# Optimization experiments

Measured on AMD Instinct MI355X. Metric: run time of the kernel, lower is better.

The kernel has to match this reference:

```python
import jax, jax.numpy as jnp
import numpy as np

NHEAD = 16


def setup_inputs() -> dict:
    key = jax.random.key(0)
    ks = jax.random.split(key, 8)
    B, T, C = 2, 1024, 2048
    H, D = NHEAD, C // NHEAD
    P = 1024  # past kv length
    s = 0.02
    return {
        "x": jax.random.normal(ks[0], (B, T, C), jnp.float32),
        "past_k": jax.random.normal(ks[1], (B, H, P, D), jnp.float32),
        "past_v": jax.random.normal(ks[2], (B, H, P, D), jnp.float32),
        "Wk": jax.random.normal(ks[3], (C, C), jnp.float32) * s,
        "Wq": jax.random.normal(ks[4], (C, C), jnp.float32) * s,
        "Wv": jax.random.normal(ks[5], (C, C), jnp.float32) * s,
        "Wp": jax.random.normal(ks[6], (C, C), jnp.float32) * s,
        "bp": jax.random.normal(ks[7], (C,), jnp.float32) * s,
    }


def reference(x, past_k, past_v, Wk, Wq, Wv, Wp, bp):
    B, T, C = x.shape
    H = NHEAD
    D = C // H
    # nn.Linear(W): y = x @ W.T ; split into heads -> [B,H,T,D]
    def proj_heads(W):
        return (x @ W.T).reshape(B, T, H, D).transpose(0, 2, 1, 3)
    q = proj_heads(Wq)
    k_new = proj_heads(Wk)
    v_new = proj_heads(Wv)
    k = jnp.concatenate([past_k, k_new], axis=2)  # [B,H,P+T,D]
    v = jnp.concatenate([past_v, v_new], axis=2)
    past_len = past_k.shape[2]
    total_len = past_len + T
    # causal mask: new-query row i attends to absolute position j <= past_len + i
    q_pos = past_len + jnp.arange(T)[:, None]        # [T,1]
    k_pos = jnp.arange(total_len)[None, :]           # [1,total]
    mask = k_pos <= q_pos                            # [T,total]
    att = jnp.einsum("bhqd,bhkd->bhqk", q, k) * (1.0 / np.sqrt(D).astype(np.float32))
    att = jnp.where(mask[None, None], att, jnp.float32(-jnp.inf))
    att = jax.nn.softmax(att, axis=-1)
    out = jnp.einsum("bhqk,bhkd->bhqd", att, v)
    out = out.transpose(0, 2, 1, 3).reshape(B, T, C)
    out = out @ Wp.T + bp
    return out, k, v
```

## Files before the change

kernel.cpp:

```cpp
#include <hip/hip_runtime.h>
#include <stdint.h>

#define B_ 2
#define T_ 1024
#define C_ 2048
#define H_ 16
#define D_ 128
#define P_ 1024
#define L_ 2048
#define M_ 2048

typedef unsigned short u16;
typedef __attribute__((ext_vector_type(8))) short short8;
typedef __attribute__((ext_vector_type(4))) float f32x4;
typedef __attribute__((ext_vector_type(8))) u16 u16x8;
typedef __attribute__((ext_vector_type(4))) u16 u16x4;

__device__ __forceinline__ u16 f2bf(float x) {
    union { float f; uint32_t u; } c; c.f = x;
    uint32_t u = c.u;
    return (u16)((u + 0x7fffu + ((u >> 16) & 1u)) >> 16);
}

__device__ __forceinline__ void gload_lds16(const void* g, void* l) {
    typedef __attribute__((address_space(1))) const void gvoid;
    typedef __attribute__((address_space(3))) void lvoid;
    __builtin_amdgcn_global_load_lds((gvoid*)g, (lvoid*)l, 16, 0, 0);
}

__global__ __launch_bounds__(256) void convert4_kernel(
        const float* __restrict__ x,  const float* __restrict__ wk,
        const float* __restrict__ wv, const float* __restrict__ wq,
        u16* __restrict__ xb, u16* __restrict__ obK,
        u16* __restrict__ obV, u16* __restrict__ obQ) {
    const int bid = blockIdx.x;
    const int r = bid >> 11;
    const int i = (bid & 2047) * 256 + threadIdx.x;
    const float* src = (r == 0) ? x : (r == 1) ? wk : (r == 2) ? wv : wq;
    u16* dst = (r == 0) ? xb : (r == 1) ? obK : (r == 2) ? obV : obQ;
    float4 a = ((const float4*)src)[i * 2], b = ((const float4*)src)[i * 2 + 1];
    ((u16x8*)dst)[i] = u16x8{f2bf(a.x), f2bf(a.y), f2bf(a.z), f2bf(a.w),
                             f2bf(b.x), f2bf(b.y), f2bf(b.z), f2bf(b.w)};
}

__global__ __launch_bounds__(256) void convert_bf16_kernel(
        const float* __restrict__ in, u16* __restrict__ out) {
    int i = blockIdx.x * 256 + threadIdx.x;
    const float4* p = (const float4*)in;
    float4 a = p[i * 2], b = p[i * 2 + 1];
    ((u16x8*)out)[i] = u16x8{f2bf(a.x), f2bf(a.y), f2bf(a.z), f2bf(a.w),
                             f2bf(b.x), f2bf(b.y), f2bf(b.z), f2bf(b.w)};
}

__global__ __launch_bounds__(256) void copy_past_kernel(
        const float4* __restrict__ pk, const float4* __restrict__ pv,
        float4* __restrict__ kdst, float4* __restrict__ vdst,
        u16x4* __restrict__ kb) {
    int i = blockIdx.x * 256 + threadIdx.x;
    int bh = i >> 15;
    int rest = i & 32767;
    size_t dst = (size_t)bh * (L_ * D_ / 4) + rest;
    float4 k4 = pk[i], v4 = pv[i];
    kdst[dst] = k4;
    vdst[dst] = v4;
    kb[dst] = u16x4{f2bf(k4.x), f2bf(k4.y), f2bf(k4.z), f2bf(k4.w)};
}

__global__ __launch_bounds__(256) void vT_past_kernel(
        const float* __restrict__ pv, u16* __restrict__ vbT) {
    __shared__ float s[64][65];
    const int tid = threadIdx.x;
    const int bh = blockIdx.x >> 5;
    const int tile = blockIdx.x & 31;
    const int k0 = (tile >> 1) * 64;
    const int d0 = (tile & 1) * 64;
    const float* src = pv + ((size_t)bh * P_ + k0) * D_ + d0;
    {
        int r = tid >> 2, c0 = (tid & 3) * 16;
#pragma unroll
        for (int u = 0; u < 4; ++u) {
            float4 f = *(const float4*)(src + (size_t)r * D_ + c0 + u * 4);
            s[r][c0 + u * 4 + 0] = f.x; s[r][c0 + u * 4 + 1] = f.y;
            s[r][c0 + u * 4 + 2] = f.z; s[r][c0 + u * 4 + 3] = f.w;
        }
    }
    __syncthreads();
    int d = tid >> 2, ck = (tid & 3) * 16;
    u16* dst = vbT + ((size_t)bh * D_ + d0 + d) * L_ + k0 + ck;
    u16x8 o0, o1;
#pragma unroll
    for (int j = 0; j < 8; ++j) o0[j] = f2bf(s[ck + j][d]);
#pragma unroll
    for (int j = 0; j < 8; ++j) o1[j] = f2bf(s[ck + 8 + j][d]);
    *(u16x8*)dst = o0;
    *(u16x8*)(dst + 8) = o1;
}

__global__ __launch_bounds__(256) void gemm_qkv(
        const u16* __restrict__ A,
        const u16* __restrict__ wbK, const u16* __restrict__ wbV,
        const u16* __restrict__ wbQ,
        float* __restrict__ kout, float* __restrict__ vout,
        u16* __restrict__ kb, u16* __restrict__ vbT, u16* __restrict__ Qst) {
    __shared__ u16 As[128 * 32];
    __shared__ u16 Bs[128 * 32];
    const int tid  = threadIdx.x;
    const int wave = tid >> 6;
    const int lane = tid & 63;
    const int m0   = blockIdx.y * 128;
    const int n0g  = blockIdx.x * 128;
    const int region = n0g >> 11;
    const int n0   = n0g & 2047;
    const u16* Bw = (region == 0) ? wbK : (region == 1) ? wbV : wbQ;

    f32x4 acc[4][4];
#pragma unroll
    for (int i = 0; i < 4; ++i)
#pragma unroll
        for (int j = 0; j < 4; ++j) acc[i][j] = f32x4{0.f, 0.f, 0.f, 0.f};

    const int srow = lane >> 2;
    const int scol = (lane & 3) * 8;
    const int q0 = wave * 2, q1 = wave * 2 + 1;
    const u16* A0 = A  + (size_t)(m0 + q0 * 16 + srow) * C_ + scol;
    const u16* A1 = A  + (size_t)(m0 + q1 * 16 + srow) * C_ + scol;
    const u16* B0 = Bw + (size_t)(n0 + q0 * 16 + srow) * C_ + scol;
    const u16* B1 = Bw + (size_t)(n0 + q1 * 16 + srow) * C_ + scol;

    const int frow = lane & 15;
    const int fko  = (lane >> 4) * 8;
    const int wr = (wave >> 1) * 64;
    const int wc = (wave & 1) * 64;

    for (int kt = 0; kt < C_; kt += 32) {
        __syncthreads();
        gload_lds16(A0 + kt, &As[q0 * 512]);
        gload_lds16(A1 + kt, &As[q1 * 512]);
        gload_lds16(B0 + kt, &Bs[q0 * 512]);
        gload_lds16(B1 + kt, &Bs[q1 * 512]);
        __syncthreads();
        short8 af[4], bf[4];
#pragma unroll
        for (int i = 0; i < 4; ++i) {
            af[i] = *(const short8*)&As[(wr + i * 16 + frow) * 32 + fko];
            bf[i] = *(const short8*)&Bs[(wc + i * 16 + frow) * 32 + fko];
        }
#pragma unroll
        for (int mi = 0; mi < 4; ++mi)
#pragma unroll
            for (int ni = 0; ni < 4; ++ni)
                acc[mi][ni] = __builtin_amdgcn_mfma_f32_16x16x32_bf16(
                    af[mi], bf[ni], acc[mi][ni], 0, 0, 0);
    }

    const int ccol = lane & 15;
    const int crb  = (lane >> 4) * 4;
#pragma unroll
    for (int mi = 0; mi < 4; ++mi) {
#pragma unroll
        for (int ni = 0; ni < 4; ++ni) {
            const int gc  = n0 + wc + ni * 16 + ccol;
            const int grb = m0 + wr + mi * 16 + crb;
            if (region == 2) {
#pragma unroll
                for (int r = 0; r < 4; ++r)
                    Qst[(size_t)(grb + r) * C_ + gc] = f2bf(acc[mi][ni][r]);
            } else {
                const int b = grb >> 10, tb = grb & 1023;
                const int h = gc >> 7,  d  = gc & 127;
                const size_t fb = (((size_t)(b * H_ + h)) * L_ + P_ + tb) * D_ + d;
                if (region == 0) {
#pragma unroll
                    for (int r = 0; r < 4; ++r) {
                        kout[fb + (size_t)r * D_] = acc[mi][ni][r];
                        kb[fb + (size_t)r * D_]   = f2bf(acc[mi][ni][r]);
                    }
                } else {
#pragma unroll
                    for (int r = 0; r < 4; ++r) vout[fb + (size_t)r * D_] = acc[mi][ni][r];
                    const size_t tb2 = (((size_t)(b * H_ + h)) * D_ + d) * L_ + P_ + tb;
                    *(u16x4*)&vbT[tb2] = u16x4{
                        f2bf(acc[mi][ni][0]), f2bf(acc[mi][ni][1]),
                        f2bf(acc[mi][ni][2]), f2bf(acc[mi][ni][3])};
                }
            }
        }
    }
}

template <int MODE>
__global__ __launch_bounds__(256) void gemm128(
        const u16* __restrict__ A, const u16* __restrict__ Bw,
        float* __restrict__ outf, u16* __restrict__ outb,
        const float* __restrict__ bias) {
    __shared__ u16 As[128 * 32];
    __shared__ u16 Bs[128 * 32];
    const int tid  = threadIdx.x;
    const int wave = tid >> 6;
    const int lane = tid & 63;
    const int m0 = blockIdx.y * 128;
    const int n0 = blockIdx.x * 128;

    f32x4 acc[4][4];
#pragma unroll
    for (int i = 0; i < 4; ++i)
#pragma unroll
        for (int j = 0; j < 4; ++j) acc[i][j] = f32x4{0.f, 0.f, 0.f, 0.f};

    const int srow = lane >> 2;
    const int scol = (lane & 3) * 8;
    const int q0 = wave * 2, q1 = wave * 2 + 1;
    const u16* A0 = A  + (size_t)(m0 + q0 * 16 + srow) * C_ + scol;
    const u16* A1 = A  + (size_t)(m0 + q1 * 16 + srow) * C_ + scol;
    const u16* B0 = Bw + (size_t)(n0 + q0 * 16 + srow) * C_ + scol;
    const u16* B1 = Bw + (size_t)(n0 + q1 * 16 + srow) * C_ + scol;

    const int frow = lane & 15;
    const int fko  = (lane >> 4) * 8;
    const int wr = (wave >> 1) * 64;
    const int wc = (wave & 1) * 64;

    for (int kt = 0; kt < C_; kt += 32) {
        __syncthreads();
        gload_lds16(A0 + kt, &As[q0 * 512]);
        gload_lds16(A1 + kt, &As[q1 * 512]);
        gload_lds16(B0 + kt, &Bs[q0 * 512]);
        gload_lds16(B1 + kt, &Bs[q1 * 512]);
        __syncthreads();
        short8 af[4], bf[4];
#pragma unroll
        for (int i = 0; i < 4; ++i) {
            af[i] = *(const short8*)&As[(wr + i * 16 + frow) * 32 + fko];
            bf[i] = *(const short8*)&Bs[(wc + i * 16 + frow) * 32 + fko];
        }
#pragma unroll
        for (int mi = 0; mi < 4; ++mi)
#pragma unroll
            for (int ni = 0; ni < 4; ++ni)
                acc[mi][ni] = __builtin_amdgcn_mfma_f32_16x16x32_bf16(
                    af[mi], bf[ni], acc[mi][ni], 0, 0, 0);
    }

    const int ccol = lane & 15;
    const int crb  = (lane >> 4) * 4;
#pragma unroll
    for (int mi = 0; mi < 4; ++mi) {
#pragma unroll
        for (int ni = 0; ni < 4; ++ni) {
            const int gc  = n0 + wc + ni * 16 + ccol;
            const int grb = m0 + wr + mi * 16 + crb;
            if (MODE == 0) {
#pragma unroll
                for (int r = 0; r < 4; ++r)
                    outb[(size_t)(grb + r) * C_ + gc] = f2bf(acc[mi][ni][r]);
            } else {
                const float ba = bias[gc];
#pragma unroll
                for (int r = 0; r < 4; ++r)
                    outf[(size_t)(grb + r) * C_ + gc] = acc[mi][ni][r] + ba;
            }
        }
    }
}

#define NEG_BIG -30000.f
__global__ __launch_bounds__(256) void attn_kernel(
        const u16* __restrict__ Q, const u16* __restrict__ Kb,
        const u16* __restrict__ VT, u16* __restrict__ O) {
    __shared__ u16 Qs[64 * 128];
    __shared__ u16 Ks[64 * 128];
    __shared__ u16 Vs[128 * 64];
    __shared__ u16 Ps[64][72];

    const int tid  = threadIdx.x;
    const int wave = tid >> 6;
    const int lane = tid & 63;
    int       qt = blockIdx.x & 15;
    const int h  = (blockIdx.x >> 4) & 15;
    const int b  = blockIdx.x >> 8;
    if (b) qt = 15 - qt;
    const int t0 = qt * 64;

    const u16* Kbase = Kb + (size_t)(b * H_ + h) * L_ * D_;
    const u16* Vbase = VT + (size_t)(b * H_ + h) * D_ * L_;

#pragma unroll
    for (int i = 0; i < 4; ++i) {
        int g   = (wave * 4 + i) * 64 + lane;
        int row = g >> 4, blk = g & 15;
        int sb  = (blk & 8) | ((blk ^ row) & 7);
        gload_lds16(Q + ((size_t)(b * T_ + t0 + row)) * C_ + h * D_ + sb * 8,
                    &Qs[(wave * 4 + i) * 512]);
    }

    const int frow = lane & 15;
    const int quad = lane >> 4;
    const int fko  = quad * 8;
    const int swz  = (frow & 7) << 3;

    f32x4 o_acc[8];
#pragma unroll
    for (int n = 0; n < 8; ++n) o_acc[n] = f32x4{0.f, 0.f, 0.f, 0.f};
    float m_i[4] = {NEG_BIG, NEG_BIG, NEG_BIG, NEG_BIG};
    float l_i[4] = {0.f, 0.f, 0.f, 0.f};
    const float scale = 0.08838834764831845f;

    const int nch = (P_ + t0 + 64) >> 6;
    const int wave_lim = P_ + t0 + wave * 16 + 15;

    for (int ch = 0; ch < nch; ++ch) {
        const int j0 = ch * 64;
        __syncthreads();
#pragma unroll
        for (int i = 0; i < 4; ++i) {
            int g = (wave * 4 + i) * 64 + lane;
            {
                int row = g >> 4, blk = g & 15;
                int sb  = (blk & 8) | ((blk ^ row) & 7);
                gload_lds16(Kbase + (size_t)(j0 + row) * D_ + sb * 8,
                            &Ks[(wave * 4 + i) * 512]);
            }
            {
                int d  = g >> 3, cb = g & 7;
                int sb = (cb ^ d) & 7;
                gload_lds16(Vbase + (size_t)d * L_ + j0 + sb * 8,
                            &Vs[(wave * 4 + i) * 512]);
            }
        }
        __syncthreads();

        const bool active = (j0 <= wave_lim);

        if (active) {
            f32x4 st[4];
#pragma unroll
            for (int j = 0; j < 4; ++j) st[j] = f32x4{0.f, 0.f, 0.f, 0.f};
            __builtin_amdgcn_s_setprio(1);
#pragma unroll
            for (int kt = 0; kt < 4; ++kt) {
                short8 a = *(const short8*)&Qs[(wave * 16 + frow) * 128 +
                                               ((kt * 32 + fko) ^ swz)];
#pragma unroll
                for (int j = 0; j < 4; ++j) {
                    short8 kf = *(const short8*)&Ks[(j * 16 + frow) * 128 +
                                                    ((kt * 32 + fko) ^ swz)];
                    st[j] = __builtin_amdgcn_mfma_f32_16x16x32_bf16(a, kf, st[j], 0, 0, 0);
                }
            }
            __builtin_amdgcn_s_setprio(0);

#pragma unroll
            for (int r = 0; r < 4; ++r) {
                const int t   = t0 + wave * 16 + quad * 4 + r;
                const int lim = P_ + t;
                float sv[4];
                float mx = NEG_BIG;
#pragma unroll
                for (int j = 0; j < 4; ++j) {
                    int jg = j0 + j * 16 + frow;
                    float s = st[j][r] * scale;
                    s = (jg <= lim) ? s : NEG_BIG;
                    sv[j] = s;
                    mx = fmaxf(mx, s);
                }
#pragma unroll
                for (int sft = 1; sft <= 8; sft <<= 1)
                    mx = fmaxf(mx, __shfl_xor(mx, sft, 64));
                const bool defer = (mx <= m_i[r] + 8.f);
                const float m_new = defer ? m_i[r] : mx;
                float rs = 0.f;
#pragma unroll
                for (int j = 0; j < 4; ++j) {
                    float p = (sv[j] <= NEG_BIG) ? 0.f : __expf(sv[j] - m_new);
                    sv[j] = p;
                    rs += p;
                }
#pragma unroll
                for (int sft = 1; sft <= 8; sft <<= 1)
                    rs += __shfl_xor(rs, sft, 64);
                if (defer) {
                    l_i[r] += rs;
                } else {
                    float alpha = __expf(fminf(m_i[r] - m_new, 0.f));
                    l_i[r] = l_i[r] * alpha + rs;
                    m_i[r] = m_new;
#pragma unroll
                    for (int n = 0; n < 8; ++n) o_acc[n][r] *= alpha;
                }
#pragma unroll
                for (int j = 0; j < 4; ++j)
                    Ps[wave * 16 + quad * 4 + r][j * 16 + frow] = f2bf(sv[j]);
            }
        }
        __syncthreads();

        if (active) {
            __builtin_amdgcn_s_setprio(1);
#pragma unroll
            for (int kt2 = 0; kt2 < 2; ++kt2) {
                short8 a = *(const short8*)&Ps[wave * 16 + frow][kt2 * 32 + fko];
#pragma unroll
                for (int n = 0; n < 8; ++n) {
                    short8 vf = *(const short8*)&Vs[(n * 16 + frow) * 64 +
                                                    ((kt2 * 32 + fko) ^ swz)];
                    o_acc[n] = __builtin_amdgcn_mfma_f32_16x16x32_bf16(a, vf, o_acc[n], 0, 0, 0);
                }
            }
            __builtin_amdgcn_s_setprio(0);
        }
    }

#pragma unroll
    for (int r = 0; r < 4; ++r) {
        float rl = 1.f / fmaxf(l_i[r], 1e-30f);
        int t = t0 + wave * 16 + quad * 4 + r;
#pragma unroll
        for (int n = 0; n < 8; ++n) {
            float v = o_acc[n][r] * rl;
            O[((size_t)(b * T_ + t)) * C_ + h * D_ + n * 16 + frow] = f2bf(v);
        }
    }
}

extern "C" void kernel_launch(void* const* d_in, const int* in_sizes, int n_in,
                              void* d_out, int out_size, void* d_ws, size_t ws_size,
                              hipStream_t stream) {
    const float* x      = (const float*)d_in[0];
    const float* past_k = (const float*)d_in[1];
    const float* past_v = (const float*)d_in[2];
    const float* Wk     = (const float*)d_in[3];
    const float* Wq     = (const float*)d_in[4];
    const float* Wv     = (const float*)d_in[5];
    const float* Wp     = (const float*)d_in[6];
    const float* bp     = (const float*)d_in[7];

    float* out  = (float*)d_out;
    float* kout = out + 4194304;
    float* vout = kout + 8388608;

    u16* Qst = (u16*)d_out;
    u16* xb  = (u16*)((char*)d_out + (8u << 20));
    u16* OstWq = (u16*)d_ws;
    u16* kb    = (u16*)((char*)d_ws + (8u  << 20));
    u16* vbT   = (u16*)((char*)d_ws + (24u << 20));
    u16* wbKP  = (u16*)((char*)d_ws + (40u << 20));
    const bool fused = ws_size >= (size_t)(56u << 20);
    u16* wbV = fused ? (u16*)((char*)d_ws + (48u << 20))
                     : Qst;

    convert4_kernel<<<8192, 256, 0, stream>>>(x, Wk, Wv, Wq, xb, wbKP, wbV, OstWq);

    copy_past_kernel<<<4096, 256, 0, stream>>>(
        (const float4*)past_k, (const float4*)past_v,
        (float4*)kout, (float4*)vout, (u16x4*)kb);
    vT_past_kernel<<<1024, 256, 0, stream>>>(past_v, vbT);

    if (fused) {
        dim3 g(48, 16);
        gemm_qkv<<<g, 256, 0, stream>>>(xb, wbKP, wbV, OstWq,
                                        kout, vout, kb, vbT, Qst);
    } else {
        dim3 gkv(32, 16);
        gemm_qkv<<<gkv, 256, 0, stream>>>(xb, wbKP, wbV, OstWq,
                                          kout, vout, kb, vbT, Qst);
        dim3 gq(16, 16);
        gemm128<0><<<gq, 256, 0, stream>>>(xb, OstWq, nullptr, Qst, nullptr);
    }

    attn_kernel<<<512, 256, 0, stream>>>(Qst, kb, vbT, OstWq);

    convert_bf16_kernel<<<2048, 256, 0, stream>>>(Wp, wbKP);
    dim3 gp(16, 16);
    gemm128<2><<<gp, 256, 0, stream>>>(OstWq, wbKP, out, nullptr, bp);
}
```

Baseline: 443.3 us.

## Fuse prep kernels, double-buffer GEMM LDS tiles, and drop deferred softmax rescale

Merges the conversion, past-KV copy and V-transpose kernels into one launch so a single grid covers all prep work. Both GEMM kernels now double-buffer their A/B LDS tiles, issuing the next k-slice's global-to-LDS loads before the current MFMAs and keeping one barrier per iteration instead of two. The attention softmax removes the lazy-rescale branch and always rescales the accumulator, trading extra multiplies for less divergence. The prep kernel now reserves 16KB of shared memory for every block, which may lower occupancy for the conversion blocks.

```diff
diff --git a/kernel.cpp b/kernel.cpp
--- a/kernel.cpp
+++ b/kernel.cpp
@@ -28,19 +28,61 @@
     __builtin_amdgcn_global_load_lds((gvoid*)g, (lvoid*)l, 16, 0, 0);
 }
 
-__global__ __launch_bounds__(256) void convert4_kernel(
+__global__ __launch_bounds__(256) void prep_kernel(
         const float* __restrict__ x,  const float* __restrict__ wk,
         const float* __restrict__ wv, const float* __restrict__ wq,
+        const float4* __restrict__ pk, const float4* __restrict__ pv,
         u16* __restrict__ xb, u16* __restrict__ obK,
-        u16* __restrict__ obV, u16* __restrict__ obQ) {
+        u16* __restrict__ obV, u16* __restrict__ obQ,
+        float4* __restrict__ kdst, float4* __restrict__ vdst,
+        u16x4* __restrict__ kb, u16* __restrict__ vbT) {
+    __shared__ float s[64][65];
     const int bid = blockIdx.x;
-    const int r = bid >> 11;
-    const int i = (bid & 2047) * 256 + threadIdx.x;
-    const float* src = (r == 0) ? x : (r == 1) ? wk : (r == 2) ? wv : wq;
-    u16* dst = (r == 0) ? xb : (r == 1) ? obK : (r == 2) ? obV : obQ;
-    float4 a = ((const float4*)src)[i * 2], b = ((const float4*)src)[i * 2 + 1];
-    ((u16x8*)dst)[i] = u16x8{f2bf(a.x), f2bf(a.y), f2bf(a.z), f2bf(a.w),
-                             f2bf(b.x), f2bf(b.y), f2bf(b.z), f2bf(b.w)};
+    const int tid = threadIdx.x;
+    if (bid < 8192) {
+        const int r = bid >> 11;
+        const int i = (bid & 2047) * 256 + tid;
+        const float* src = (r == 0) ? x : (r == 1) ? wk : (r == 2) ? wv : wq;
+        u16* dst = (r == 0) ? xb : (r == 1) ? obK : (r == 2) ? obV : obQ;
+        float4 a = ((const float4*)src)[i * 2], b = ((const float4*)src)[i * 2 + 1];
+        ((u16x8*)dst)[i] = u16x8{f2bf(a.x), f2bf(a.y), f2bf(a.z), f2bf(a.w),
+                                 f2bf(b.x), f2bf(b.y), f2bf(b.z), f2bf(b.w)};
+    } else if (bid < 12288) {
+        const int i = (bid - 8192) * 256 + tid;
+        const int bh = i >> 15;
+        const int rest = i & 32767;
+        const size_t dst = (size_t)bh * (L_ * D_ / 4) + rest;
+        float4 k4 = pk[i], v4 = pv[i];
+        kdst[dst] = k4;
+        vdst[dst] = v4;
+        kb[dst] = u16x4{f2bf(k4.x), f2bf(k4.y), f2bf(k4.z), f2bf(k4.w)};
+    } else {
+        const int tb = bid - 12288;
+        const int bh = tb >> 5;
+        const int tile = tb & 31;
+        const int k0 = (tile >> 1) * 64;
+        const int d0 = (tile & 1) * 64;
+        const float* src = (const float*)pv + ((size_t)bh * P_ + k0) * D_ + d0;
+        {
+            int r = tid >> 2, c0 = (tid & 3) * 16;
+#pragma unroll
+            for (int u = 0; u < 4; ++u) {
+                float4 f = *(const float4*)(src + (size_t)r * D_ + c0 + u * 4);
+                s[r][c0 + u * 4 + 0] = f.x; s[r][c0 + u * 4 + 1] = f.y;
+                s[r][c0 + u * 4 + 2] = f.z; s[r][c0 + u * 4 + 3] = f.w;
+            }
+        }
+        __syncthreads();
+        int d = tid >> 2, ck = (tid & 3) * 16;
+        u16* dst = vbT + ((size_t)bh * D_ + d0 + d) * L_ + k0 + ck;
+        u16x8 o0, o1;
+#pragma unroll
+        for (int j = 0; j < 8; ++j) o0[j] = f2bf(s[ck + j][d]);
+#pragma unroll
+        for (int j = 0; j < 8; ++j) o1[j] = f2bf(s[ck + 8 + j][d]);
+        *(u16x8*)dst = o0;
+        *(u16x8*)(dst + 8) = o1;
+    }
 }
 
 __global__ __launch_bounds__(256) void convert_bf16_kernel(
@@ -52,58 +94,14 @@
                              f2bf(b.x), f2bf(b.y), f2bf(b.z), f2bf(b.w)};
 }
 
-__global__ __launch_bounds__(256) void copy_past_kernel(
-        const float4* __restrict__ pk, const float4* __restrict__ pv,
-        float4* __restrict__ kdst, float4* __restrict__ vdst,
-        u16x4* __restrict__ kb) {
-    int i = blockIdx.x * 256 + threadIdx.x;
-    int bh = i >> 15;
-    int rest = i & 32767;
-    size_t dst = (size_t)bh * (L_ * D_ / 4) + rest;
-    float4 k4 = pk[i], v4 = pv[i];
-    kdst[dst] = k4;
-    vdst[dst] = v4;
-    kb[dst] = u16x4{f2bf(k4.x), f2bf(k4.y), f2bf(k4.z), f2bf(k4.w)};
-}
-
-__global__ __launch_bounds__(256) void vT_past_kernel(
-        const float* __restrict__ pv, u16* __restrict__ vbT) {
-    __shared__ float s[64][65];
-    const int tid = threadIdx.x;
-    const int bh = blockIdx.x >> 5;
-    const int tile = blockIdx.x & 31;
-    const int k0 = (tile >> 1) * 64;
-    const int d0 = (tile & 1) * 64;
-    const float* src = pv + ((size_t)bh * P_ + k0) * D_ + d0;
-    {
-        int r = tid >> 2, c0 = (tid & 3) * 16;
-#pragma unroll
-        for (int u = 0; u < 4; ++u) {
-            float4 f = *(const float4*)(src + (size_t)r * D_ + c0 + u * 4);
-            s[r][c0 + u * 4 + 0] = f.x; s[r][c0 + u * 4 + 1] = f.y;
-            s[r][c0 + u * 4 + 2] = f.z; s[r][c0 + u * 4 + 3] = f.w;
-        }
-    }
-    __syncthreads();
-    int d = tid >> 2, ck = (tid & 3) * 16;
-    u16* dst = vbT + ((size_t)bh * D_ + d0 + d) * L_ + k0 + ck;
-    u16x8 o0, o1;
-#pragma unroll
-    for (int j = 0; j < 8; ++j) o0[j] = f2bf(s[ck + j][d]);
-#pragma unroll
-    for (int j = 0; j < 8; ++j) o1[j] = f2bf(s[ck + 8 + j][d]);
-    *(u16x8*)dst = o0;
-    *(u16x8*)(dst + 8) = o1;
-}
-
 __global__ __launch_bounds__(256) void gemm_qkv(
         const u16* __restrict__ A,
         const u16* __restrict__ wbK, const u16* __restrict__ wbV,
         const u16* __restrict__ wbQ,
         float* __restrict__ kout, float* __restrict__ vout,
         u16* __restrict__ kb, u16* __restrict__ vbT, u16* __restrict__ Qst) {
-    __shared__ u16 As[128 * 32];
-    __shared__ u16 Bs[128 * 32];
+    __shared__ u16 As[2][128 * 32];
+    __shared__ u16 Bs[2][128 * 32];
     const int tid  = threadIdx.x;
     const int wave = tid >> 6;
     const int lane = tid & 63;
@@ -132,18 +130,26 @@
     const int wr = (wave >> 1) * 64;
     const int wc = (wave & 1) * 64;
 
+    gload_lds16(A0, &As[0][q0 * 512]);
+    gload_lds16(A1, &As[0][q1 * 512]);
+    gload_lds16(B0, &Bs[0][q0 * 512]);
+    gload_lds16(B1, &Bs[0][q1 * 512]);
+    __syncthreads();
+
+    int cur = 0;
     for (int kt = 0; kt < C_; kt += 32) {
-        __syncthreads();
-        gload_lds16(A0 + kt, &As[q0 * 512]);
-        gload_lds16(A1 + kt, &As[q1 * 512]);
-        gload_lds16(B0 + kt, &Bs[q0 * 512]);
-        gload_lds16(B1 + kt, &Bs[q1 * 512]);
-        __syncthreads();
+        const int nxt = cur ^ 1;
+        if (kt + 32 < C_) {
+            gload_lds16(A0 + kt + 32, &As[nxt][q0 * 512]);
+            gload_lds16(A1 + kt + 32, &As[nxt][q1 * 512]);
+            gload_lds16(B0 + kt + 32, &Bs[nxt][q0 * 512]);
+            gload_lds16(B1 + kt + 32, &Bs[nxt][q1 * 512]);
+        }
         short8 af[4], bf[4];
 #pragma unroll
         for (int i = 0; i < 4; ++i) {
-            af[i] = *(const short8*)&As[(wr + i * 16 + frow) * 32 + fko];
-            bf[i] = *(const short8*)&Bs[(wc + i * 16 + frow) * 32 + fko];
+            af[i] = *(const short8*)&As[cur][(wr + i * 16 + frow) * 32 + fko];
+            bf[i] = *(const short8*)&Bs[cur][(wc + i * 16 + frow) * 32 + fko];
         }
 #pragma unroll
         for (int mi = 0; mi < 4; ++mi)
@@ -151,6 +157,8 @@
             for (int ni = 0; ni < 4; ++ni)
                 acc[mi][ni] = __builtin_amdgcn_mfma_f32_16x16x32_bf16(
                     af[mi], bf[ni], acc[mi][ni], 0, 0, 0);
+        __syncthreads();
+        cur = nxt;
     }
 
     const int ccol = lane & 15;
@@ -193,8 +201,8 @@
         const u16* __restrict__ A, const u16* __restrict__ Bw,
         float* __restrict__ outf, u16* __restrict__ outb,
         const float* __restrict__ bias) {
-    __shared__ u16 As[128 * 32];
-    __shared__ u16 Bs[128 * 32];
+    __shared__ u16 As[2][128 * 32];
+    __shared__ u16 Bs[2][128 * 32];
     const int tid  = threadIdx.x;
     const int wave = tid >> 6;
     const int lane = tid & 63;
@@ -220,18 +228,26 @@
     const int wr = (wave >> 1) * 64;
     const int wc = (wave & 1) * 64;
 
+    gload_lds16(A0, &As[0][q0 * 512]);
+    gload_lds16(A1, &As[0][q1 * 512]);
+    gload_lds16(B0, &Bs[0][q0 * 512]);
+    gload_lds16(B1, &Bs[0][q1 * 512]);
+    __syncthreads();
+
+    int cur = 0;
     for (int kt = 0; kt < C_; kt += 32) {
-        __syncthreads();
-        gload_lds16(A0 + kt, &As[q0 * 512]);
-        gload_lds16(A1 + kt, &As[q1 * 512]);
-        gload_lds16(B0 + kt, &Bs[q0 * 512]);
-        gload_lds16(B1 + kt, &Bs[q1 * 512]);
-        __syncthreads();
+        const int nxt = cur ^ 1;
+        if (kt + 32 < C_) {
+            gload_lds16(A0 + kt + 32, &As[nxt][q0 * 512]);
+            gload_lds16(A1 + kt + 32, &As[nxt][q1 * 512]);
+            gload_lds16(B0 + kt + 32, &Bs[nxt][q0 * 512]);
+            gload_lds16(B1 + kt + 32, &Bs[nxt][q1 * 512]);
+        }
         short8 af[4], bf[4];
 #pragma unroll
         for (int i = 0; i < 4; ++i) {
-            af[i] = *(const short8*)&As[(wr + i * 16 + frow) * 32 + fko];
-            bf[i] = *(const short8*)&Bs[(wc + i * 16 + frow) * 32 + fko];
+            af[i] = *(const short8*)&As[cur][(wr + i * 16 + frow) * 32 + fko];
+            bf[i] = *(const short8*)&Bs[cur][(wc + i * 16 + frow) * 32 + fko];
         }
 #pragma unroll
         for (int mi = 0; mi < 4; ++mi)
@@ -239,6 +255,8 @@
             for (int ni = 0; ni < 4; ++ni)
                 acc[mi][ni] = __builtin_amdgcn_mfma_f32_16x16x32_bf16(
                     af[mi], bf[ni], acc[mi][ni], 0, 0, 0);
+        __syncthreads();
+        cur = nxt;
     }
 
     const int ccol = lane & 15;
@@ -366,27 +384,23 @@
 #pragma unroll
                 for (int sft = 1; sft <= 8; sft <<= 1)
                     mx = fmaxf(mx, __shfl_xor(mx, sft, 64));
-                const bool defer = (mx <= m_i[r] + 8.f);
-                const float m_new = defer ? m_i[r] : mx;
+                float m_new = fmaxf(m_i[r], mx);
+                float alpha = __expf(fminf(m_i[r] - m_new, 0.f));
                 float rs = 0.f;
 #pragma unroll
                 for (int j = 0; j < 4; ++j) {
-                    float p = (sv[j] <= NEG_BIG) ? 0.f : __expf(sv[j] - m_new);
+                    float p = __expf(fminf(sv[j] - m_new, 0.f));
+                    p = (sv[j] <= NEG_BIG) ? 0.f : p;
                     sv[j] = p;
                     rs += p;
                 }
 #pragma unroll
                 for (int sft = 1; sft <= 8; sft <<= 1)
                     rs += __shfl_xor(rs, sft, 64);
-                if (defer) {
-                    l_i[r] += rs;
-                } else {
-                    float alpha = __expf(fminf(m_i[r] - m_new, 0.f));
-                    l_i[r] = l_i[r] * alpha + rs;
-                    m_i[r] = m_new;
-#pragma unroll
-                    for (int n = 0; n < 8; ++n) o_acc[n][r] *= alpha;
-                }
+                l_i[r] = l_i[r] * alpha + rs;
+                m_i[r] = m_new;
+#pragma unroll
+                for (int n = 0; n < 8; ++n) o_acc[n][r] *= alpha;
 #pragma unroll
                 for (int j = 0; j < 4; ++j)
                     Ps[wave * 16 + quad * 4 + r][j * 16 + frow] = f2bf(sv[j]);
@@ -448,12 +462,11 @@
     u16* wbV = fused ? (u16*)((char*)d_ws + (48u << 20))
                      : Qst;
 
-    convert4_kernel<<<8192, 256, 0, stream>>>(x, Wk, Wv, Wq, xb, wbKP, wbV, OstWq);
-
-    copy_past_kernel<<<4096, 256, 0, stream>>>(
+    prep_kernel<<<13312, 256, 0, stream>>>(
+        x, Wk, Wv, Wq,
         (const float4*)past_k, (const float4*)past_v,
-        (float4*)kout, (float4*)vout, (u16x4*)kb);
-    vT_past_kernel<<<1024, 256, 0, stream>>>(past_v, vbT);
+        xb, wbKP, wbV, OstWq,
+        (float4*)kout, (float4*)vout, (u16x4*)kb, vbT);
 
     if (fused) {
         dim3 g(48, 16);
```

Result: faster. 420.5 us (-5.1%).
